# Performance work log

Hardware: AMD Instinct MI355X
Metric: run time of the kernel (lower is better)

Reference implementation:

```python
import jax, jax.numpy as jnp
import numpy as np

NUM_GROUPS = 512   # G: number of FPS centers
GROUP_SIZE = 32    # K: neighbors per group


def setup_inputs() -> dict:
    key = jax.random.key(0)
    points = jax.random.normal(key, (16, 8192, 6), dtype=jnp.float32)  # [B,N,C], xyz = first 3 ch
    return {"points": points}


def _farthest_point_sampling(xyz, K):
    """Iterative FPS. xyz: [B,N,3] -> indices [B,K] (int32).

    Deterministic start at index 0 (the torch module uses a random start; we fix
    it for a reproducible reference -- the math per step is identical).
    """
    B, N, _ = xyz.shape
    start = jnp.zeros((B,), dtype=jnp.int32)
    min_d = jnp.full((B, N), jnp.inf, dtype=xyz.dtype)

    def step(carry, _):
        min_d, last = carry
        last_pt = jnp.take_along_axis(xyz, last[:, None, None], axis=1)  # [B,1,3]
        d = jnp.sum((xyz - last_pt) ** 2, axis=-1)                       # [B,N]
        min_d = jnp.minimum(min_d, d)
        nxt = jnp.argmax(min_d, axis=-1).astype(jnp.int32)
        return (min_d, nxt), last

    _, idxs = jax.lax.scan(step, (min_d, start), None, length=K)
    return jnp.transpose(idxs)  # [B,K]


def reference(points):
    xyz = points[:, :, :3]                                   # [B,N,3]
    fps_idx = _farthest_point_sampling(xyz, NUM_GROUPS)      # [B,G]
    centers = jnp.take_along_axis(xyz, fps_idx[:, :, None], axis=1)  # [B,G,3]

    # Squared pairwise distances [B,G,N] via expanded GEMM (compute-dominant part).
    d2 = (jnp.sum(centers * centers, axis=-1)[:, :, None]
          - 2.0 * jnp.einsum('bgc,bnc->bgn', centers, xyz)
          + jnp.sum(xyz * xyz, axis=-1)[:, None, :])

    # KNN: smallest K distances (torch uses return_sorted=False; ordering of the
    # K neighbors is irrelevant to the grouping semantics).
    _, knn_idx = jax.lax.top_k(-d2, GROUP_SIZE)              # [B,G,K]

    # knn_gather: [B,N,C] gathered by [B,G,K] -> [B,G,K,C]
    grouped = jax.vmap(lambda p, i: p[i])(points, knn_idx)

    # Center-subtract on xyz channels only.
    grouped = jnp.concatenate(
        [grouped[..., :3] - centers[:, :, None, :], grouped[..., 3:]], axis=-1)
    return grouped, centers
```

## Files before the change

### kernel.cpp

```cpp
#include <hip/hip_runtime.h>
#include <hip/hip_bf16.h>
#include <stdint.h>

#define BATCH 16
#define NPTS  8192
#define NCH   6
#define NGRP  512
#define GSZ   32

#define FPS_T   1024
#define FPS_PPT 8
#define FPS_W   16

typedef float v2f __attribute__((ext_vector_type(2)));

template <int CTRL>
__device__ __forceinline__ float dpp_max_f32(float v) {
  const int t =
      __builtin_amdgcn_update_dpp(0, __float_as_int(v), CTRL, 0xf, 0xf, true);
  return fmaxf(v, __int_as_float(t));
}

template <int CTRL>
__device__ __forceinline__ unsigned dpp_min_u32(unsigned v) {
  const int t = __builtin_amdgcn_update_dpp((int)0xFFFFFFFF, (int)v, CTRL,
                                            0xf, 0xf, false);
  const unsigned tu = (unsigned)t;
  return v < tu ? v : tu;
}

__global__ __launch_bounds__(FPS_T, 1) void fps_kernel(
    const float* __restrict__ points, float* __restrict__ centers) {
#pragma clang fp contract(off)
  const int b    = blockIdx.x;
  const int tid  = threadIdx.x;
  const int lane = tid & 63;
  const int wave = tid >> 6;
  const float* P = points + (size_t)b * NPTS * NCH;
  float* C = centers + (size_t)b * NGRP * 3;

  __shared__ float cache[NPTS * 3];
  __shared__ unsigned long long wslot[2][FPS_W];

  v2f px[4], py[4], pz[4], md[4];
  {
    float* fx = (float*)px; float* fy = (float*)py; float* fz = (float*)pz;
#pragma unroll
    for (int j = 0; j < FPS_PPT; ++j) {
      const int i = tid * FPS_PPT + j;
      const float x = P[i * 6 + 0];
      const float y = P[i * 6 + 1];
      const float z = P[i * 6 + 2];
      fx[j] = x; fy[j] = y; fz[j] = z;
      cache[i * 3 + 0] = x;
      cache[i * 3 + 1] = y;
      cache[i * 3 + 2] = z;
    }
#pragma unroll
    for (int j = 0; j < 4; ++j) md[j] = (v2f){__builtin_inff(), __builtin_inff()};
  }
  __syncthreads();

  float lx = cache[0], ly = cache[1], lz = cache[2];

  for (int k = 1; k < NGRP; ++k) {
    if (tid == 0) {
      C[(k - 1) * 3 + 0] = lx; C[(k - 1) * 3 + 1] = ly; C[(k - 1) * 3 + 2] = lz;
    }

    const v2f vlx = {lx, lx}, vly = {ly, ly}, vlz = {lz, lz};
    v2f b2 = {-__builtin_inff(), -__builtin_inff()};
#pragma unroll
    for (int j = 0; j < 4; ++j) {
      const v2f dx = px[j] - vlx;
      const v2f dy = py[j] - vly;
      const v2f dz = pz[j] - vlz;
      const v2f d  = (dx * dx + dy * dy) + dz * dz;
      md[j] = __builtin_elementwise_min(md[j], d);
      b2 = __builtin_elementwise_max(b2, md[j]);
    }
    const float bestv = fmaxf(b2.x, b2.y);

    unsigned idxbest = 0;
#pragma unroll
    for (int j = 3; j >= 0; --j) {
      idxbest = (md[j].y == bestv) ? (unsigned)(tid * 8 + 2 * j + 1) : idxbest;
      idxbest = (md[j].x == bestv) ? (unsigned)(tid * 8 + 2 * j)     : idxbest;
    }

    float wv = bestv;
    wv = dpp_max_f32<0x111>(wv); wv = dpp_max_f32<0x112>(wv);
    wv = dpp_max_f32<0x114>(wv); wv = dpp_max_f32<0x118>(wv);
    wv = dpp_max_f32<0x142>(wv); wv = dpp_max_f32<0x143>(wv);
    const float wvmax =
        __int_as_float(__builtin_amdgcn_readlane(__float_as_int(wv), 63));

    const unsigned long long m1 = __ballot(bestv == wvmax);
    const int owner = (int)__builtin_ctzll(m1);
    if (lane == owner)
      wslot[k & 1][wave] =
          ((unsigned long long)__float_as_uint(wvmax) << 32) | idxbest;
    __syncthreads();

    const unsigned long long slot = wslot[k & 1][lane & 15];
    const unsigned sidx = (unsigned)(slot & 0xFFFFFFFFull);
    const float    sval = __uint_as_float((unsigned)(slot >> 32));
    const float ccx = cache[sidx * 3 + 0];
    const float ccy = cache[sidx * 3 + 1];
    const float ccz = cache[sidx * 3 + 2];

    float r = sval;
    r = dpp_max_f32<0x111>(r); r = dpp_max_f32<0x112>(r);
    r = dpp_max_f32<0x114>(r); r = dpp_max_f32<0x118>(r);
    const float gmax =
        __int_as_float(__builtin_amdgcn_readlane(__float_as_int(r), 15));
    const int sstar =
        (int)__builtin_ctzll(__ballot(sval == gmax) & 0xFFFFull);
    lx = __int_as_float(__builtin_amdgcn_readlane(__float_as_int(ccx), sstar));
    ly = __int_as_float(__builtin_amdgcn_readlane(__float_as_int(ccy), sstar));
    lz = __int_as_float(__builtin_amdgcn_readlane(__float_as_int(ccz), sstar));
  }
  if (tid == 0) {
    C[(NGRP - 1) * 3 + 0] = lx;
    C[(NGRP - 1) * 3 + 1] = ly;
    C[(NGRP - 1) * 3 + 2] = lz;
  }
}

__global__ __launch_bounds__(256) void knn_kernel(
    const float* __restrict__ points, const float* __restrict__ centers,
    float* __restrict__ grouped) {
#pragma clang fp contract(off)
  const int g    = blockIdx.x;
  const int b    = blockIdx.y;
  const int tid  = threadIdx.x;
  const int lane = tid & 63;
  const int wave = tid >> 6;
  const float* P   = points + (size_t)b * NPTS * NCH;
  const float* cen = centers + ((size_t)b * NGRP + g) * 3;
  const float cx = cen[0], cy = cen[1], cz = cen[2];
  const float cc = (cx * cx + cy * cy) + cz * cz;

  unsigned long long keys[32];
  for (int j = 0; j < 32; ++j) {
    const int i = j * 256 + tid;
    const float x = P[i * 6 + 0];
    const float y = P[i * 6 + 1];
    const float z = P[i * 6 + 2];
    const float xx  = (x * x + y * y) + z * z;
    const float dot = fmaf(cz, z, fmaf(cy, y, cx * x));
    const float d2  = (cc - 2.0f * dot) + xx;
    unsigned u = __float_as_uint(d2);
    u = (u & 0x80000000u) ? ~u : (u | 0x80000000u);
    keys[j] = ((unsigned long long)u << 32) | (unsigned long long)(unsigned)i;
  }
  unsigned long long lmin = keys[0];
  for (int j = 1; j < 32; ++j) lmin = lmin < keys[j] ? lmin : keys[j];

  __shared__ unsigned long long wred[2][4];
  __shared__ int knn_sh[GSZ];

  for (int j = 0; j < GSZ; ++j) {
    const unsigned vcur = (unsigned)(lmin >> 32);
    const unsigned icur = (unsigned)(lmin & 0xFFFFFFFFull);
    unsigned vm = vcur;
    vm = dpp_min_u32<0x111>(vm); vm = dpp_min_u32<0x112>(vm);
    vm = dpp_min_u32<0x114>(vm); vm = dpp_min_u32<0x118>(vm);
    vm = dpp_min_u32<0x142>(vm); vm = dpp_min_u32<0x143>(vm);
    const unsigned vmin =
        (unsigned)__builtin_amdgcn_readlane((int)vm, 63);
    unsigned ic = (vcur == vmin) ? icur : 0xFFFFFFFFu;
    ic = dpp_min_u32<0x111>(ic); ic = dpp_min_u32<0x112>(ic);
    ic = dpp_min_u32<0x114>(ic); ic = dpp_min_u32<0x118>(ic);
    ic = dpp_min_u32<0x142>(ic); ic = dpp_min_u32<0x143>(ic);
    const unsigned imin =
        (unsigned)__builtin_amdgcn_readlane((int)ic, 63);

    if (lane == 0)
      wred[j & 1][wave] =
          ((unsigned long long)vmin << 32) | (unsigned long long)imin;
    __syncthreads();
    unsigned long long w = wred[j & 1][0];
    for (int q2 = 1; q2 < 4; ++q2) {
      const unsigned long long o = wred[j & 1][q2];
      w = w < o ? w : o;
    }
    const int widx = (int)(unsigned)(w & 0xFFFFFFFFull);
    if (tid == (widx & 255)) {
      for (int s = 0; s < 32; ++s)
        if ((unsigned)(keys[s] & 0xFFFFFFFFull) == (unsigned)widx)
          keys[s] = ~0ull;
      lmin = keys[0];
      for (int s = 1; s < 32; ++s) lmin = lmin < keys[s] ? lmin : keys[s];
    }
    if (tid == 0) knn_sh[j] = widx;
  }
  __syncthreads();

  float* outg = grouped + ((size_t)b * NGRP + g) * GSZ * NCH;
  for (int t = tid; t < GSZ * NCH; t += 256) {
    const int n = t / 6, c = t % 6;
    const int idx = knn_sh[n];
    float v = P[idx * 6 + c];
    if (c < 3) v = v - cen[c];
    outg[t] = v;
  }
}

extern "C" void kernel_launch(void* const* d_in, const int* in_sizes, int n_in,
                              void* d_out, int out_size, void* d_ws, size_t ws_size,
                              hipStream_t stream) {
  const float* points = (const float*)d_in[0];
  float* out = (float*)d_out;
  float* grouped = out;
  float* centers = out + (size_t)BATCH * NGRP * GSZ * NCH;

  fps_kernel<<<BATCH, FPS_T, 0, stream>>>(points, centers);
  knn_kernel<<<dim3(NGRP, BATCH), 256, 0, stream>>>(points, centers, grouped);
}
```

Measured before the change: 805.7 us.

## Split FPS per batch across four cooperating blocks with global-memory handshake

```diff
diff --git a/kernel.cpp b/kernel.cpp
--- a/kernel.cpp
+++ b/kernel.cpp
@@ -8,9 +8,10 @@
 #define NGRP  512
 #define GSZ   32
 
-#define FPS_T   1024
-#define FPS_PPT 8
-#define FPS_W   16
+#define FPS_T  1024
+#define FPS_Q  4
+#define FPS_W  16
+#define PPB    (NPTS / FPS_Q)
 
 typedef float v2f __attribute__((ext_vector_type(2)));
 
@@ -30,63 +31,43 @@
 }
 
 __global__ __launch_bounds__(FPS_T, 1) void fps_kernel(
-    const float* __restrict__ points, float* __restrict__ centers) {
+    const float* __restrict__ points, float* __restrict__ centers,
+    unsigned* __restrict__ ws) {
 #pragma clang fp contract(off)
-  const int b    = blockIdx.x;
+  const int b    = blockIdx.x & 15;
+  const int q    = blockIdx.x >> 4;
   const int tid  = threadIdx.x;
   const int lane = tid & 63;
   const int wave = tid >> 6;
   const float* P = points + (size_t)b * NPTS * NCH;
   float* C = centers + (size_t)b * NGRP * 3;
 
-  __shared__ float cache[NPTS * 3];
   __shared__ unsigned long long wslot[2][FPS_W];
-
-  v2f px[4], py[4], pz[4], md[4];
-  {
-    float* fx = (float*)px; float* fy = (float*)py; float* fz = (float*)pz;
-#pragma unroll
-    for (int j = 0; j < FPS_PPT; ++j) {
-      const int i = tid * FPS_PPT + j;
-      const float x = P[i * 6 + 0];
-      const float y = P[i * 6 + 1];
-      const float z = P[i * 6 + 2];
-      fx[j] = x; fy[j] = y; fz[j] = z;
-      cache[i * 3 + 0] = x;
-      cache[i * 3 + 1] = y;
-      cache[i * 3 + 2] = z;
-    }
-#pragma unroll
-    for (int j = 0; j < 4; ++j) md[j] = (v2f){__builtin_inff(), __builtin_inff()};
-  }
-  __syncthreads();
-
-  float lx = cache[0], ly = cache[1], lz = cache[2];
+  __shared__ float bc[2][3];
+
+  const int i0 = q * PPB + tid * 2;
+  v2f px, py, pz, md;
+  px.x = P[i0 * 6 + 0];       py.x = P[i0 * 6 + 1];       pz.x = P[i0 * 6 + 2];
+  px.y = P[(i0 + 1) * 6 + 0]; py.y = P[(i0 + 1) * 6 + 1]; pz.y = P[(i0 + 1) * 6 + 2];
+  md = (v2f){__builtin_inff(), __builtin_inff()};
+
+  float lx = P[0], ly = P[1], lz = P[2];
 
   for (int k = 1; k < NGRP; ++k) {
-    if (tid == 0) {
+    if (q == 0 && tid == 0) {
       C[(k - 1) * 3 + 0] = lx; C[(k - 1) * 3 + 1] = ly; C[(k - 1) * 3 + 2] = lz;
     }
 
     const v2f vlx = {lx, lx}, vly = {ly, ly}, vlz = {lz, lz};
-    v2f b2 = {-__builtin_inff(), -__builtin_inff()};
-#pragma unroll
-    for (int j = 0; j < 4; ++j) {
-      const v2f dx = px[j] - vlx;
-      const v2f dy = py[j] - vly;
-      const v2f dz = pz[j] - vlz;
-      const v2f d  = (dx * dx + dy * dy) + dz * dz;
-      md[j] = __builtin_elementwise_min(md[j], d);
-      b2 = __builtin_elementwise_max(b2, md[j]);
-    }
-    const float bestv = fmaxf(b2.x, b2.y);
-
+    const v2f dx = px - vlx;
+    const v2f dy = py - vly;
+    const v2f dz = pz - vlz;
+    const v2f d  = (dx * dx + dy * dy) + dz * dz;
+    md = __builtin_elementwise_min(md, d);
+    const float bestv = fmaxf(md.x, md.y);
     unsigned idxbest = 0;
-#pragma unroll
-    for (int j = 3; j >= 0; --j) {
-      idxbest = (md[j].y == bestv) ? (unsigned)(tid * 8 + 2 * j + 1) : idxbest;
-      idxbest = (md[j].x == bestv) ? (unsigned)(tid * 8 + 2 * j)     : idxbest;
-    }
+    idxbest = (md.y == bestv) ? (unsigned)(i0 + 1) : idxbest;
+    idxbest = (md.x == bestv) ? (unsigned)i0       : idxbest;
 
     float wv = bestv;
     wv = dpp_max_f32<0x111>(wv); wv = dpp_max_f32<0x112>(wv);
@@ -94,21 +75,16 @@
     wv = dpp_max_f32<0x142>(wv); wv = dpp_max_f32<0x143>(wv);
     const float wvmax =
         __int_as_float(__builtin_amdgcn_readlane(__float_as_int(wv), 63));
-
-    const unsigned long long m1 = __ballot(bestv == wvmax);
-    const int owner = (int)__builtin_ctzll(m1);
+    const int owner = (int)__builtin_ctzll(__ballot(bestv == wvmax));
+
+    const int p = k & 1;
     if (lane == owner)
-      wslot[k & 1][wave] =
+      wslot[p][wave] =
           ((unsigned long long)__float_as_uint(wvmax) << 32) | idxbest;
     __syncthreads();
 
-    const unsigned long long slot = wslot[k & 1][lane & 15];
-    const unsigned sidx = (unsigned)(slot & 0xFFFFFFFFull);
-    const float    sval = __uint_as_float((unsigned)(slot >> 32));
-    const float ccx = cache[sidx * 3 + 0];
-    const float ccy = cache[sidx * 3 + 1];
-    const float ccz = cache[sidx * 3 + 2];
-
+    const unsigned long long slot = wslot[p][lane & 15];
+    const float sval = __uint_as_float((unsigned)(slot >> 32));
     float r = sval;
     r = dpp_max_f32<0x111>(r); r = dpp_max_f32<0x112>(r);
     r = dpp_max_f32<0x114>(r); r = dpp_max_f32<0x118>(r);
@@ -116,11 +92,65 @@
         __int_as_float(__builtin_amdgcn_readlane(__float_as_int(r), 15));
     const int sstar =
         (int)__builtin_ctzll(__ballot(sval == gmax) & 0xFFFFull);
-    lx = __int_as_float(__builtin_amdgcn_readlane(__float_as_int(ccx), sstar));
-    ly = __int_as_float(__builtin_amdgcn_readlane(__float_as_int(ccy), sstar));
-    lz = __int_as_float(__builtin_amdgcn_readlane(__float_as_int(ccz), sstar));
-  }
-  if (tid == 0) {
+
+    if (wave == sstar && lane == owner) {
+      float fx = 0.f, fy = 0.f, fz = 0.f;
+      if (md.y == bestv) { fx = px.y; fy = py.y; fz = pz.y; }
+      if (md.x == bestv) { fx = px.x; fy = py.x; fz = pz.x; }
+      unsigned* g = ws + (((unsigned)(b * FPS_Q + q) * 2u + (unsigned)p) * 8u);
+      __hip_atomic_store(g + 2, __float_as_uint(fx), __ATOMIC_RELAXED,
+                         __HIP_MEMORY_SCOPE_AGENT);
+      __hip_atomic_store(g + 3, __float_as_uint(fy), __ATOMIC_RELAXED,
+                         __HIP_MEMORY_SCOPE_AGENT);
+      __hip_atomic_store(g + 4, __float_as_uint(fz), __ATOMIC_RELAXED,
+                         __HIP_MEMORY_SCOPE_AGENT);
+      const unsigned long long key =
+          ((unsigned long long)__float_as_uint(wvmax) << 32) |
+          ((unsigned)k << 13) | idxbest;
+      __hip_atomic_store((unsigned long long*)g, key, __ATOMIC_RELEASE,
+                         __HIP_MEMORY_SCOPE_AGENT);
+    }
+
+    if (wave == 0) {
+      unsigned long long kk = 0ull, kk0;
+      float wxr = 0.f, wyr = 0.f, wzr = 0.f;
+      if (lane < FPS_Q) {
+        unsigned* g =
+            ws + (((unsigned)(b * FPS_Q + lane) * 2u + (unsigned)p) * 8u);
+        unsigned long long key;
+        for (;;) {
+          key = __hip_atomic_load((unsigned long long*)g, __ATOMIC_ACQUIRE,
+                                  __HIP_MEMORY_SCOPE_AGENT);
+          if ((unsigned)((key & 0xFFFFFFFFull) >> 13) == (unsigned)k) break;
+        }
+        wxr = __uint_as_float(__hip_atomic_load(g + 2, __ATOMIC_RELAXED,
+                                                __HIP_MEMORY_SCOPE_AGENT));
+        wyr = __uint_as_float(__hip_atomic_load(g + 3, __ATOMIC_RELAXED,
+                                                __HIP_MEMORY_SCOPE_AGENT));
+        wzr = __uint_as_float(__hip_atomic_load(g + 4, __ATOMIC_RELAXED,
+                                                __HIP_MEMORY_SCOPE_AGENT));
+        const unsigned idx = (unsigned)key & 0x1FFFu;
+        const unsigned val = (unsigned)(key >> 32);
+        kk = ((unsigned long long)val << 32) |
+             (unsigned long long)(8191u - idx);
+      }
+      kk0 = kk;
+      { const unsigned long long o = __shfl_xor(kk, 1); kk = kk > o ? kk : o; }
+      { const unsigned long long o = __shfl_xor(kk, 2); kk = kk > o ? kk : o; }
+      const int wl =
+          (int)__builtin_ctzll(__ballot(lane < FPS_Q && kk0 == kk));
+      const float bx =
+          __uint_as_float(__builtin_amdgcn_readlane(__float_as_int(wxr), wl));
+      const float by =
+          __uint_as_float(__builtin_amdgcn_readlane(__float_as_int(wyr), wl));
+      const float bz =
+          __uint_as_float(__builtin_amdgcn_readlane(__float_as_int(wzr), wl));
+      if (lane == 0) { bc[p][0] = bx; bc[p][1] = by; bc[p][2] = bz; }
+    }
+    __syncthreads();
+    lx = bc[p][0]; ly = bc[p][1]; lz = bc[p][2];
+  }
+  if (q == 0 && tid == 0) {
     C[(NGRP - 1) * 3 + 0] = lx;
     C[(NGRP - 1) * 3 + 1] = ly;
     C[(NGRP - 1) * 3 + 2] = lz;
@@ -167,14 +197,12 @@
     vm = dpp_min_u32<0x111>(vm); vm = dpp_min_u32<0x112>(vm);
     vm = dpp_min_u32<0x114>(vm); vm = dpp_min_u32<0x118>(vm);
     vm = dpp_min_u32<0x142>(vm); vm = dpp_min_u32<0x143>(vm);
-    const unsigned vmin =
-        (unsigned)__builtin_amdgcn_readlane((int)vm, 63);
+    const unsigned vmin = (unsigned)__builtin_amdgcn_readlane((int)vm, 63);
     unsigned ic = (vcur == vmin) ? icur : 0xFFFFFFFFu;
     ic = dpp_min_u32<0x111>(ic); ic = dpp_min_u32<0x112>(ic);
     ic = dpp_min_u32<0x114>(ic); ic = dpp_min_u32<0x118>(ic);
     ic = dpp_min_u32<0x142>(ic); ic = dpp_min_u32<0x143>(ic);
-    const unsigned imin =
-        (unsigned)__builtin_amdgcn_readlane((int)ic, 63);
+    const unsigned imin = (unsigned)__builtin_amdgcn_readlane((int)ic, 63);
 
     if (lane == 0)
       wred[j & 1][wave] =
@@ -214,7 +242,8 @@
   float* out = (float*)d_out;
   float* grouped = out;
   float* centers = out + (size_t)BATCH * NGRP * GSZ * NCH;
-
-  fps_kernel<<<BATCH, FPS_T, 0, stream>>>(points, centers);
+  unsigned* ws = (unsigned*)d_ws;
+
+  fps_kernel<<<BATCH * FPS_Q, FPS_T, 0, stream>>>(points, centers, ws);
   knn_kernel<<<dim3(NGRP, BATCH), 256, 0, stream>>>(points, centers, grouped);
 }
```

New measurement: 1.885 ms. 2.34x slower.

## Replace FPS per-iteration barrier with tagged LDS flags and spin-wait

Applied to the files above, without the earlier changes.

```diff
diff --git a/kernel.cpp b/kernel.cpp
--- a/kernel.cpp
+++ b/kernel.cpp
@@ -40,7 +40,8 @@
   float* C = centers + (size_t)b * NGRP * 3;
 
   __shared__ float cache[NPTS * 3];
-  __shared__ unsigned long long wslot[2][FPS_W];
+  __shared__ unsigned long long wdata[2][FPS_W];
+  __shared__ unsigned wtag[2][FPS_W];
 
   v2f px[4], py[4], pz[4], md[4];
   {
@@ -59,6 +60,7 @@
 #pragma unroll
     for (int j = 0; j < 4; ++j) md[j] = (v2f){__builtin_inff(), __builtin_inff()};
   }
+  if (tid < 32) wtag[tid >> 4][tid & 15] = 0;
   __syncthreads();
 
   float lx = cache[0], ly = cache[1], lz = cache[2];
@@ -94,15 +96,27 @@
     wv = dpp_max_f32<0x142>(wv); wv = dpp_max_f32<0x143>(wv);
     const float wvmax =
         __int_as_float(__builtin_amdgcn_readlane(__float_as_int(wv), 63));
-
-    const unsigned long long m1 = __ballot(bestv == wvmax);
-    const int owner = (int)__builtin_ctzll(m1);
-    if (lane == owner)
-      wslot[k & 1][wave] =
-          ((unsigned long long)__float_as_uint(wvmax) << 32) | idxbest;
-    __syncthreads();
-
-    const unsigned long long slot = wslot[k & 1][lane & 15];
+    const int owner = (int)__builtin_ctzll(__ballot(bestv == wvmax));
+
+    const int p = k & 1;
+    if (lane == owner) {
+      __hip_atomic_store(&wdata[p][wave],
+                         ((unsigned long long)__float_as_uint(wvmax) << 32) |
+                             idxbest,
+                         __ATOMIC_RELAXED, __HIP_MEMORY_SCOPE_WORKGROUP);
+      __hip_atomic_store(&wtag[p][wave], (unsigned)k, __ATOMIC_RELEASE,
+                         __HIP_MEMORY_SCOPE_WORKGROUP);
+    }
+
+    unsigned tg;
+    do {
+      tg = __hip_atomic_load(&wtag[p][lane & 15], __ATOMIC_ACQUIRE,
+                             __HIP_MEMORY_SCOPE_WORKGROUP);
+    } while (__ballot(tg == (unsigned)k) != ~0ull);
+
+    const unsigned long long slot =
+        __hip_atomic_load(&wdata[p][lane & 15], __ATOMIC_RELAXED,
+                          __HIP_MEMORY_SCOPE_WORKGROUP);
     const unsigned sidx = (unsigned)(slot & 0xFFFFFFFFull);
     const float    sval = __uint_as_float((unsigned)(slot >> 32));
     const float ccx = cache[sidx * 3 + 0];
@@ -167,14 +181,12 @@
     vm = dpp_min_u32<0x111>(vm); vm = dpp_min_u32<0x112>(vm);
     vm = dpp_min_u32<0x114>(vm); vm = dpp_min_u32<0x118>(vm);
     vm = dpp_min_u32<0x142>(vm); vm = dpp_min_u32<0x143>(vm);
-    const unsigned vmin =
-        (unsigned)__builtin_amdgcn_readlane((int)vm, 63);
+    const unsigned vmin = (unsigned)__builtin_amdgcn_readlane((int)vm, 63);
     unsigned ic = (vcur == vmin) ? icur : 0xFFFFFFFFu;
     ic = dpp_min_u32<0x111>(ic); ic = dpp_min_u32<0x112>(ic);
     ic = dpp_min_u32<0x114>(ic); ic = dpp_min_u32<0x118>(ic);
     ic = dpp_min_u32<0x142>(ic); ic = dpp_min_u32<0x143>(ic);
-    const unsigned imin =
-        (unsigned)__builtin_amdgcn_readlane((int)ic, 63);
+    const unsigned imin = (unsigned)__builtin_amdgcn_readlane((int)ic, 63);
 
     if (lane == 0)
       wred[j & 1][wave] =
```

Result: slower. 824.2 us (+2.3%).

## Per-wave independent top-32 selection with bitonic merge instead of block-synced rounds

Applied to the files above, without the earlier changes.

```diff
diff --git a/kernel.cpp b/kernel.cpp
--- a/kernel.cpp
+++ b/kernel.cpp
@@ -142,10 +142,11 @@
   const float cc = (cx * cx + cy * cy) + cz * cz;
 
   unsigned long long keys[32];
+#pragma unroll
   for (int j = 0; j < 32; ++j) {
     const int i = j * 256 + tid;
-    const float x = P[i * 6 + 0];
-    const float y = P[i * 6 + 1];
+    const float2 xy = *reinterpret_cast<const float2*>(P + (size_t)i * 6);
+    const float x = xy.x, y = xy.y;
     const float z = P[i * 6 + 2];
     const float xx  = (x * x + y * y) + z * z;
     const float dot = fmaf(cz, z, fmaf(cy, y, cx * x));
@@ -154,55 +155,104 @@
     u = (u & 0x80000000u) ? ~u : (u | 0x80000000u);
     keys[j] = ((unsigned long long)u << 32) | (unsigned long long)(unsigned)i;
   }
-  unsigned long long lmin = keys[0];
-  for (int j = 1; j < 32; ++j) lmin = lmin < keys[j] ? lmin : keys[j];
-
-  __shared__ unsigned long long wred[2][4];
+
+  unsigned long long gm[4];
+#pragma unroll
+  for (int g2 = 0; g2 < 4; ++g2) {
+    unsigned long long m = keys[g2 * 8];
+#pragma unroll
+    for (int t = 1; t < 8; ++t) {
+      const unsigned long long o = keys[g2 * 8 + t];
+      m = m < o ? m : o;
+    }
+    gm[g2] = m;
+  }
+  unsigned long long lmin;
+  {
+    const unsigned long long a2 = gm[0] < gm[1] ? gm[0] : gm[1];
+    const unsigned long long b3 = gm[2] < gm[3] ? gm[2] : gm[3];
+    lmin = a2 < b3 ? a2 : b3;
+  }
+
+  __shared__ unsigned long long wtop[4][GSZ];
   __shared__ int knn_sh[GSZ];
 
-  for (int j = 0; j < GSZ; ++j) {
+  for (int r2 = 0; r2 < GSZ; ++r2) {
     const unsigned vcur = (unsigned)(lmin >> 32);
     const unsigned icur = (unsigned)(lmin & 0xFFFFFFFFull);
     unsigned vm = vcur;
     vm = dpp_min_u32<0x111>(vm); vm = dpp_min_u32<0x112>(vm);
     vm = dpp_min_u32<0x114>(vm); vm = dpp_min_u32<0x118>(vm);
     vm = dpp_min_u32<0x142>(vm); vm = dpp_min_u32<0x143>(vm);
-    const unsigned vmin =
-        (unsigned)__builtin_amdgcn_readlane((int)vm, 63);
+    const unsigned vmin = (unsigned)__builtin_amdgcn_readlane((int)vm, 63);
     unsigned ic = (vcur == vmin) ? icur : 0xFFFFFFFFu;
     ic = dpp_min_u32<0x111>(ic); ic = dpp_min_u32<0x112>(ic);
     ic = dpp_min_u32<0x114>(ic); ic = dpp_min_u32<0x118>(ic);
     ic = dpp_min_u32<0x142>(ic); ic = dpp_min_u32<0x143>(ic);
-    const unsigned imin =
-        (unsigned)__builtin_amdgcn_readlane((int)ic, 63);
-
-    if (lane == 0)
-      wred[j & 1][wave] =
-          ((unsigned long long)vmin << 32) | (unsigned long long)imin;
-    __syncthreads();
-    unsigned long long w = wred[j & 1][0];
-    for (int q2 = 1; q2 < 4; ++q2) {
-      const unsigned long long o = wred[j & 1][q2];
-      w = w < o ? w : o;
-    }
-    const int widx = (int)(unsigned)(w & 0xFFFFFFFFull);
-    if (tid == (widx & 255)) {
-      for (int s = 0; s < 32; ++s)
-        if ((unsigned)(keys[s] & 0xFFFFFFFFull) == (unsigned)widx)
-          keys[s] = ~0ull;
-      lmin = keys[0];
-      for (int s = 1; s < 32; ++s) lmin = lmin < keys[s] ? lmin : keys[s];
-    }
-    if (tid == 0) knn_sh[j] = widx;
+    const unsigned imin = (unsigned)__builtin_amdgcn_readlane((int)ic, 63);
+    const unsigned long long wk =
+        ((unsigned long long)vmin << 32) | (unsigned long long)imin;
+
+    if (lane == (int)(imin & 63u)) {
+#pragma unroll
+      for (int g2 = 0; g2 < 4; ++g2) {
+        if (gm[g2] == wk) {
+          unsigned long long m = ~0ull;
+#pragma unroll
+          for (int t = 0; t < 8; ++t) {
+            const int s = g2 * 8 + t;
+            if (keys[s] == wk) keys[s] = ~0ull;
+            const unsigned long long o = keys[s];
+            m = m < o ? m : o;
+          }
+          gm[g2] = m;
+        }
+      }
+      const unsigned long long a2 = gm[0] < gm[1] ? gm[0] : gm[1];
+      const unsigned long long b3 = gm[2] < gm[3] ? gm[2] : gm[3];
+      lmin = a2 < b3 ? a2 : b3;
+    }
+    if (lane == 0) wtop[wave][r2] = wk;
+  }
+  __syncthreads();
+
+  if (wave == 0) {
+    const unsigned long long* flat = &wtop[0][0];
+    unsigned long long a = flat[lane];
+    unsigned long long c = flat[lane + 64];
+#pragma unroll
+    for (int k2 = 2; k2 <= 128; k2 <<= 1) {
+#pragma unroll
+      for (int j2 = k2 >> 1; j2 >= 1; j2 >>= 1) {
+        if (j2 == 64) {
+          const unsigned long long mn = a < c ? a : c;
+          const unsigned long long mx = a < c ? c : a;
+          a = mn; c = mx;
+        } else {
+          const bool upa = ((lane & k2) == 0);
+          const bool upc = (((lane + 64) & k2) == 0);
+          const unsigned long long oa = __shfl_xor(a, j2);
+          const unsigned long long oc = __shfl_xor(c, j2);
+          const bool low = ((lane & j2) == 0);
+          const unsigned long long mna = a < oa ? a : oa;
+          const unsigned long long mxa = a < oa ? oa : a;
+          const unsigned long long mnc = c < oc ? c : oc;
+          const unsigned long long mxc = c < oc ? oc : c;
+          a = (low == upa) ? mna : mxa;
+          c = (low == upc) ? mnc : mxc;
+        }
+      }
+    }
+    if (lane < GSZ) knn_sh[lane] = (int)(unsigned)(a & 0xFFFFFFFFull);
   }
   __syncthreads();
 
   float* outg = grouped + ((size_t)b * NGRP + g) * GSZ * NCH;
   for (int t = tid; t < GSZ * NCH; t += 256) {
-    const int n = t / 6, c = t % 6;
+    const int n = t / 6, c2 = t % 6;
     const int idx = knn_sh[n];
-    float v = P[idx * 6 + c];
-    if (c < 3) v = v - cen[c];
+    float v = P[idx * 6 + c2];
+    if (c2 < 3) v = v - cen[c2];
     outg[t] = v;
   }
 }
```

Result: faster. 741.7 us (-7.9%).
